# Kernel optimization log

Hardware: AMD Instinct MI355X
Metric: run time of the kernel (lower is better)

## Reference

```python
import jax, jax.numpy as jnp
import numpy as np
from jax import lax

H = W = 128          # feature map size (gen_line_map uses 128x128)
C = 128              # dim_loi
NPTS0 = 32           # n_pts0 samples per line
NPTS1 = 8            # after MaxPool1d(4, stride=4)
TOPK = 50            # n_dyn_junc
SCALE = 5.0          # proposal_lines distance scale


def proposal_lines(md_maps, dis_maps, scale=SCALE):
    h, w = md_maps.shape[1], md_maps.shape[2]
    y0, x0 = jnp.meshgrid(jnp.arange(h, dtype=jnp.float32),
                          jnp.arange(w, dtype=jnp.float32), indexing='ij')
    md_ = (md_maps[0] - 0.5) * np.pi * 2
    st_ = md_maps[1] * np.pi / 2
    ed_ = -md_maps[2] * np.pi / 2
    cs_md, ss_md = jnp.cos(md_), jnp.sin(md_)
    cs_st = jnp.clip(jnp.cos(st_), 0.001, None)
    ss_st = jnp.clip(jnp.sin(st_), 0.001, None)
    cs_ed = jnp.clip(jnp.cos(ed_), 0.001, None)
    ss_ed = jnp.clip(jnp.sin(ed_), None, -0.001)
    y_st = ss_st / cs_st
    y_ed = ss_ed / cs_ed
    d = dis_maps[0] * scale
    x_st = (cs_md - ss_md * y_st) * d
    y_s = (ss_md + cs_md * y_st) * d
    x_ed = (cs_md - ss_md * y_ed) * d
    y_e = (ss_md + cs_md * y_ed) * d
    x_st_f = jnp.clip(x_st + x0, 0.0, w - 1)
    y_st_f = jnp.clip(y_s + y0, 0.0, h - 1)
    x_ed_f = jnp.clip(x_ed + x0, 0.0, w - 1)
    y_ed_f = jnp.clip(y_e + y0, 0.0, h - 1)
    return jnp.stack((x_st_f, y_st_f, x_ed_f, y_ed_f), axis=-1).reshape(-1, 4)


def pooling(feats, lines):
    # feats: [C, H, W]; lines: [N, 4]
    h, w = feats.shape[1], feats.shape[2]
    tspan = jnp.linspace(0.0, 1.0, NPTS0)[None, None, :]           # [1,1,32]
    U, V = lines[:, :2], lines[:, 2:]
    sp = U[:, :, None] * tspan + V[:, :, None] * (1 - tspan) - 0.5  # [N,2,32]
    sp = sp.transpose(0, 2, 1).reshape(-1, 2)                       # [N*32, 2]
    px, py = sp[:, 0], sp[:, 1]
    px0 = jnp.clip(jnp.floor(px), 0.0, w - 1)
    py0 = jnp.clip(jnp.floor(py), 0.0, h - 1)
    px1 = jnp.clip(px0 + 1, 0.0, w - 1)
    py1 = jnp.clip(py0 + 1, 0.0, h - 1)
    px0l, py0l = px0.astype(jnp.int32), py0.astype(jnp.int32)
    px1l, py1l = px1.astype(jnp.int32), py1.astype(jnp.int32)
    # bilinear gather-weight, fused in a single expression: [C, N*32]
    xp = (feats[:, py0l, px0l] * (py1 - py) * (px1 - px)
          + feats[:, py1l, px0l] * (py - py0) * (px1 - px)
          + feats[:, py0l, px1l] * (py1 - py) * (px - px0)
          + feats[:, py1l, px1l] * (py - py0) * (px - px0))
    xp = xp.reshape(C, -1, NPTS0).transpose(1, 0, 2)                # [N, C, 32]
    xp = xp.reshape(xp.shape[0], C, NPTS1, NPTS0 // NPTS1).max(-1)  # MaxPool1d(4,4)
    return xp.reshape(-1, NPTS1 * C)                                # [N, 1024]


def nms(a):
    # F.max_pool2d(a, 3, stride=1, padding=1) then keep local maxima
    ap = lax.reduce_window(a, -jnp.inf, lax.max, (1, 3, 3), (1, 1, 1), 'SAME')
    return a * (a == ap).astype(a.dtype)


def get_junctions(jloc_nms, joff, topk=TOPK):
    h, w = jloc_nms.shape[1], jloc_nms.shape[2]
    scores, index = lax.top_k(jloc_nms.reshape(-1), topk)
    jf = joff.reshape(2, -1)
    y = (index // w).astype(jnp.float32) + jf[1][index] + 0.5
    x = (index % w).astype(jnp.float32) + jf[0][index] + 0.5
    juncs = jnp.stack((x, y), axis=1)                               # [topk, 2]
    return juncs, scores, index


def setup_inputs() -> dict:
    key = jax.random.key(0)
    ks = jax.random.split(key, 12)
    return {
        'md': jax.random.uniform(ks[0], (3, H, W), dtype=jnp.float32),
        'dis': jax.random.uniform(ks[1], (1, H, W), dtype=jnp.float32),
        'res': jax.random.uniform(ks[2], (1, H, W), dtype=jnp.float32),
        'jloc': jax.random.uniform(ks[3], (1, H, W), dtype=jnp.float32),
        'joff': jax.random.uniform(ks[4], (2, H, W), dtype=jnp.float32) - 0.5,
        'feats': jax.random.normal(ks[5], (C, H, W), dtype=jnp.float32),
        'W1': jax.random.normal(ks[6], (1024, C * NPTS1), dtype=jnp.float32) * 0.02,
        'b1': jax.random.normal(ks[7], (1024,), dtype=jnp.float32) * 0.02,
        'W2': jax.random.normal(ks[8], (1024, 1024), dtype=jnp.float32) * 0.02,
        'b2': jax.random.normal(ks[9], (1024,), dtype=jnp.float32) * 0.02,
        'W3': jax.random.normal(ks[10], (1, 1024), dtype=jnp.float32) * 0.02,
        'b3': jax.random.normal(ks[11], (1,), dtype=jnp.float32) * 0.02,
    }


def reference(md, dis, res, jloc, joff, feats, W1, b1, W2, b2, W3, b3):
    # line proposals at 3 residual scales (use_residual=True)
    lines = jnp.concatenate([
        proposal_lines(md, dis + s * res) for s in (-1.0, 0.0, 1.0)
    ], axis=0)                                                      # [3*H*W, 4]
    # LOI bilinear pooling + scoring MLP (self.fc)
    x = pooling(feats, lines)                                       # [N, 1024]
    x = jax.nn.relu(x @ W1.T + b1)
    x = jax.nn.relu(x @ W2.T + b2)
    logits = x @ W3.T + b3                                          # [N, 1]
    # junction decode: NMS + topk + offset gather
    juncs, jscores, _ = get_junctions(nms(jloc), joff, TOPK)
    return logits, juncs, jscores
```

## Files before the change

kernel.cpp:

```cpp
#include <hip/hip_runtime.h>
#include <hip/hip_bf16.h>
#include <math.h>

#define HH 128
#define WW 128
#define HW 16384
#define NL 49152
#define CC 128
#define NPTS0 32
#define NPTS1 8
#define PI_F 3.14159265358979323846f

typedef __attribute__((ext_vector_type(8))) short short8;
typedef __attribute__((ext_vector_type(4))) float f32x4;

__device__ __forceinline__ ushort f2bf(float f) {
    unsigned u = __builtin_bit_cast(unsigned, f);
    unsigned rounding = 0x7FFFu + ((u >> 16) & 1u);
    return (ushort)((u + rounding) >> 16);
}

__device__ __forceinline__ void gload_lds16(const void* gsrc, void* ldst) {
    __builtin_amdgcn_global_load_lds(
        (const __attribute__((address_space(1))) unsigned int*)gsrc,
        (__attribute__((address_space(3))) unsigned int*)ldst,
        16, 0, 0);
}

__device__ __forceinline__ void unpk8(uint4 d, float* f) {
    f[0] = __builtin_bit_cast(float, d.x << 16);
    f[1] = __builtin_bit_cast(float, d.x & 0xFFFF0000u);
    f[2] = __builtin_bit_cast(float, d.y << 16);
    f[3] = __builtin_bit_cast(float, d.y & 0xFFFF0000u);
    f[4] = __builtin_bit_cast(float, d.z << 16);
    f[5] = __builtin_bit_cast(float, d.z & 0xFFFF0000u);
    f[6] = __builtin_bit_cast(float, d.w << 16);
    f[7] = __builtin_bit_cast(float, d.w & 0xFFFF0000u);
}

__global__ __launch_bounds__(256) void k_lines(
    const float* __restrict__ md, const float* __restrict__ dis,
    const float* __restrict__ res, float* __restrict__ lines)
{
    int g = blockIdx.x * 256 + threadIdx.x;
    if (g >= NL) return;
    int s = g / HW;
    int pix = g - s * HW;
    float sf = (float)(s - 1);
    int y = pix >> 7, x = pix & 127;

    float md0 = md[pix], md1 = md[HW + pix], md2 = md[2 * HW + pix];
    float d = (dis[pix] + sf * res[pix]) * 5.0f;

    float md_ = (md0 - 0.5f) * (2.0f * PI_F);
    float st_ = md1 * (0.5f * PI_F);
    float ed_ = -md2 * (0.5f * PI_F);
    float cs_md = cosf(md_), ss_md = sinf(md_);
    float cs_st = fmaxf(cosf(st_), 0.001f);
    float ss_st = fmaxf(sinf(st_), 0.001f);
    float cs_ed = fmaxf(cosf(ed_), 0.001f);
    float ss_ed = fminf(sinf(ed_), -0.001f);
    float y_st = ss_st / cs_st;
    float y_ed = ss_ed / cs_ed;
    float x_st = (cs_md - ss_md * y_st) * d;
    float y_s  = (ss_md + cs_md * y_st) * d;
    float x_ed = (cs_md - ss_md * y_ed) * d;
    float y_e  = (ss_md + cs_md * y_ed) * d;

    float4 o;
    o.x = fminf(fmaxf(x_st + (float)x, 0.0f), 127.0f);
    o.y = fminf(fmaxf(y_s  + (float)y, 0.0f), 127.0f);
    o.z = fminf(fmaxf(x_ed + (float)x, 0.0f), 127.0f);
    o.w = fminf(fmaxf(y_e  + (float)y, 0.0f), 127.0f);
    ((float4*)lines)[g] = o;
}

__global__ void k_transpose(const float* __restrict__ in, ushort* __restrict__ out)
{
    __shared__ float tile[32][33];
    int cb = blockIdx.x;
    int pb = blockIdx.y;
    int tx = threadIdx.x, ty = threadIdx.y;
#pragma unroll
    for (int j = 0; j < 32; j += 8)
        tile[ty + j][tx] = in[(size_t)(cb * 32 + ty + j) * HW + pb * 32 + tx];
    __syncthreads();
#pragma unroll
    for (int j = 0; j < 32; j += 8)
        out[(size_t)(pb * 32 + ty + j) * CC + cb * 32 + tx] = f2bf(tile[tx][ty + j]);
}

__global__ void k_cvt(const float* __restrict__ a, const float* __restrict__ b,
                      ushort* __restrict__ oa, ushort* __restrict__ ob, int n)
{
    int i = blockIdx.x * 256 + threadIdx.x;
    if (i < n) { oa[i] = f2bf(a[i]); ob[i] = f2bf(b[i]); }
}

__global__ __launch_bounds__(128, 4) void k_pool(
    const ushort* __restrict__ ft, const float* __restrict__ lines,
    ushort* __restrict__ X)
{
    __shared__ __align__(16) unsigned smeta[2048];
    const int t = threadIdx.x;
    const int l_loc = t >> 4, c8 = t & 15;
    const int gl0 = blockIdx.x * 8;

#pragma unroll
    for (int e = 0; e < 2; ++e) {
        int s = t + e * 128;
        int ml = s >> 5, sp = s & 31;
        float4 L = ((const float4*)lines)[gl0 + ml];
        float tf = (float)sp * (1.0f / 31.0f);
        float omt = 1.0f - tf;
        float px = L.x * tf + L.z * omt - 0.5f;
        float py = L.y * tf + L.w * omt - 0.5f;
        float px0 = fminf(fmaxf(floorf(px), 0.0f), 127.0f);
        float py0 = fminf(fmaxf(floorf(py), 0.0f), 127.0f);
        float px1 = fminf(px0 + 1.0f, 127.0f);
        float py1 = fminf(py0 + 1.0f, 127.0f);
        int ix0 = (int)px0, iy0 = (int)py0, ix1 = (int)px1, iy1 = (int)py1;
        float4 wv;
        wv.x = (py1 - py) * (px1 - px);
        wv.y = (py  - py0) * (px1 - px);
        wv.z = (py1 - py) * (px  - px0);
        wv.w = (py  - py0) * (px  - px0);
        int o00 = (iy0 * WW + ix0) * (CC * 2);
        int dx  = (ix1 - ix0) * (CC * 2);
        int dy  = (iy1 - iy0) * (WW * CC * 2);
        int4 ov;
        ov.x = o00;
        ov.y = o00 + dy;
        ov.z = o00 + dx;
        ov.w = o00 + dy + dx;
        *(float4*)&smeta[s * 8]     = wv;
        *(int4*)  &smeta[s * 8 + 4] = ov;
    }
    __syncthreads();

    const unsigned coff = (unsigned)(c8 * 16);
    const char* fbase = (const char*)ft;
    float m[8][8];
#pragma unroll
    for (int ch = 0; ch < 8; ++ch)
#pragma unroll
        for (int g = 0; g < 8; ++g) m[ch][g] = -INFINITY;

#pragma unroll
    for (int g = 0; g < 8; ++g) {
#pragma unroll
        for (int j = 0; j < 4; ++j) {
            const unsigned* mp = &smeta[(l_loc * 32 + g * 4 + j) * 8];
            float4 wv = *(const float4*)mp;
            int4  ov = *(const int4*)(mp + 4);
            uint4 d00 = *(const uint4*)(fbase + ((unsigned)ov.x + coff));
            uint4 d10 = *(const uint4*)(fbase + ((unsigned)ov.y + coff));
            uint4 d01 = *(const uint4*)(fbase + ((unsigned)ov.z + coff));
            uint4 d11 = *(const uint4*)(fbase + ((unsigned)ov.w + coff));
            float f00[8], f10[8], f01[8], f11[8];
            unpk8(d00, f00); unpk8(d10, f10); unpk8(d01, f01); unpk8(d11, f11);
#pragma unroll
            for (int ch = 0; ch < 8; ++ch) {
                float v = f00[ch] * wv.x + f10[ch] * wv.y
                        + f01[ch] * wv.z + f11[ch] * wv.w;
                m[ch][g] = fmaxf(m[ch][g], v);
            }
        }
    }

    ushort* Xp = X + (size_t)(gl0 + l_loc) * 1024 + c8 * 64;
#pragma unroll
    for (int ch = 0; ch < 8; ++ch) {
        short8 pk;
#pragma unroll
        for (int g = 0; g < 8; ++g) pk[g] = (short)f2bf(m[ch][g]);
        *(short8*)(Xp + ch * 8) = pk;
    }
}

#define NT 32
template<int EPI>
__global__ __launch_bounds__(512, 2) void k_gemm2(
    const ushort* __restrict__ A, const ushort* __restrict__ B,
    const float* __restrict__ bias, ushort* __restrict__ Y,
    const float* __restrict__ w3, float* __restrict__ logits,
    int M, int N, int K)
{
    __shared__ __align__(16) ushort lds[65536];
    const int tid = threadIdx.x;
    const int w = tid >> 6, l = tid & 63;
    const int lr = l & 15, kq = l >> 4;
    const int wm = w >> 2, wn = w & 3;

    const int nwg = gridDim.x;
    const int cpx = nwg >> 3;
    const int swz = (blockIdx.x & 7) * cpx + (blockIdx.x >> 3);
    const int nbm = M >> 8;
    const int m_blk = swz % nbm;
    const int n_blk = swz / nbm;
    const int m0 = m_blk << 8, n0 = n_blk << 8;

    const int G0 = tid, G1 = 512 + tid;
    const int r0 = G0 >> 2, r1 = G1 >> 2;
    const int g0 = (G0 & 3) ^ ((r0 >> 1) & 3);
    const int g1 = (G1 & 3) ^ ((r1 >> 1) & 3);
    const ushort* sA0 = A + (size_t)(m0 + r0) * K + g0 * 8;
    const ushort* sA1 = A + (size_t)(m0 + r1) * K + g1 * 8;
    const ushort* sB0 = B + (size_t)(n0 + r0) * K + g0 * 8;
    const ushort* sB1 = B + (size_t)(n0 + r1) * K + g1 * 8;
    ushort* dA0 = &lds[G0 * 8];
    ushort* dA1 = &lds[G1 * 8];
    ushort* dB0 = &lds[32768 + G0 * 8];
    ushort* dB1 = &lds[32768 + G1 * 8];

#define STAGE_A(tp) { int sb = ((tp) & 3) * 8192; \
    gload_lds16(sA0 + (tp) * 32, dA0 + sb); \
    gload_lds16(sA1 + (tp) * 32, dA1 + sb); }
#define STAGE_B(tp) { int sb = ((tp) & 3) * 8192; \
    gload_lds16(sB0 + (tp) * 32, dB0 + sb); \
    gload_lds16(sB1 + (tp) * 32, dB1 + sb); }
#define SBAR  { __builtin_amdgcn_sched_barrier(0); __builtin_amdgcn_s_barrier(); \
                __builtin_amdgcn_sched_barrier(0); }

    int aidx[8], bidx[4];
#pragma unroll
    for (int m = 0; m < 8; ++m) {
        int r = wm * 128 + m * 16 + lr;
        int g = kq ^ ((r >> 1) & 3);
        aidx[m] = r * 32 + g * 8;
    }
#pragma unroll
    for (int n = 0; n < 4; ++n) {
        int r = wn * 64 + n * 16 + lr;
        int g = kq ^ ((r >> 1) & 3);
        bidx[n] = 32768 + r * 32 + g * 8;
    }

    f32x4 acc[8][4] = {};

    STAGE_A(0); STAGE_B(0); STAGE_A(1); STAGE_B(1); STAGE_A(2);
    asm volatile("s_waitcnt vmcnt(6)" ::: "memory");
    SBAR;

    for (int t = 0; t < NT; ++t) {
        const int sb = (t & 3) * 8192;
        short8 bq0 = *(const short8*)&lds[sb + bidx[0]];
        short8 bq1 = *(const short8*)&lds[sb + bidx[1]];
        short8 bq2 = *(const short8*)&lds[sb + bidx[2]];
        short8 bq3 = *(const short8*)&lds[sb + bidx[3]];
        short8 a0 = *(const short8*)&lds[sb + aidx[0]];
        short8 a1 = *(const short8*)&lds[sb + aidx[1]];
        short8 a2 = *(const short8*)&lds[sb + aidx[2]];
        short8 a3 = *(const short8*)&lds[sb + aidx[3]];
        if (t + 2 < NT) STAGE_B(t + 2);
        __builtin_amdgcn_s_setprio(1);
#pragma unroll
        for (int n = 0; n < 4; ++n) {
            short8 bn = (n == 0) ? bq0 : (n == 1) ? bq1 : (n == 2) ? bq2 : bq3;
            acc[0][n] = __builtin_amdgcn_mfma_f32_16x16x32_bf16(a0, bn, acc[0][n], 0, 0, 0);
            acc[1][n] = __builtin_amdgcn_mfma_f32_16x16x32_bf16(a1, bn, acc[1][n], 0, 0, 0);
            acc[2][n] = __builtin_amdgcn_mfma_f32_16x16x32_bf16(a2, bn, acc[2][n], 0, 0, 0);
            acc[3][n] = __builtin_amdgcn_mfma_f32_16x16x32_bf16(a3, bn, acc[3][n], 0, 0, 0);
        }
        __builtin_amdgcn_s_setprio(0);
        SBAR;
        short8 a4 = *(const short8*)&lds[sb + aidx[4]];
        short8 a5 = *(const short8*)&lds[sb + aidx[5]];
        short8 a6 = *(const short8*)&lds[sb + aidx[6]];
        short8 a7 = *(const short8*)&lds[sb + aidx[7]];
        if (t + 3 < NT) STAGE_A(t + 3);
        __builtin_amdgcn_s_setprio(1);
#pragma unroll
        for (int n = 0; n < 4; ++n) {
            short8 bn = (n == 0) ? bq0 : (n == 1) ? bq1 : (n == 2) ? bq2 : bq3;
            acc[4][n] = __builtin_amdgcn_mfma_f32_16x16x32_bf16(a4, bn, acc[4][n], 0, 0, 0);
            acc[5][n] = __builtin_amdgcn_mfma_f32_16x16x32_bf16(a5, bn, acc[5][n], 0, 0, 0);
            acc[6][n] = __builtin_amdgcn_mfma_f32_16x16x32_bf16(a6, bn, acc[6][n], 0, 0, 0);
            acc[7][n] = __builtin_amdgcn_mfma_f32_16x16x32_bf16(a7, bn, acc[7][n], 0, 0, 0);
        }
        __builtin_amdgcn_s_setprio(0);
        if (t < NT - 3) {
            asm volatile("s_waitcnt vmcnt(6)" ::: "memory");
        } else {
            asm volatile("s_waitcnt vmcnt(0)" ::: "memory");
        }
        SBAR;
    }
#undef STAGE_A
#undef STAGE_B
#undef SBAR

    if (EPI == 0) {
        float bv[4];
#pragma unroll
        for (int n = 0; n < 4; ++n) bv[n] = bias[n0 + wn * 64 + n * 16 + lr];
#pragma unroll
        for (int m = 0; m < 8; ++m) {
#pragma unroll
            for (int n = 0; n < 4; ++n) {
                int col = n0 + wn * 64 + n * 16 + lr;
#pragma unroll
                for (int j = 0; j < 4; ++j) {
                    int row = m0 + wm * 128 + m * 16 + kq * 4 + j;
                    float v = fmaxf(acc[m][n][j] + bv[n], 0.0f);
                    Y[(size_t)row * N + col] = f2bf(v);
                }
            }
        }
    } else {
        float w3v[4], bv[4];
#pragma unroll
        for (int n = 0; n < 4; ++n) {
            int col = n0 + wn * 64 + n * 16 + lr;
            w3v[n] = w3[col];
            bv[n] = bias[col];
        }
#pragma unroll
        for (int m = 0; m < 8; ++m) {
#pragma unroll
            for (int j = 0; j < 4; ++j) {
                float s = 0.0f;
#pragma unroll
                for (int n = 0; n < 4; ++n)
                    s += fmaxf(acc[m][n][j] + bv[n], 0.0f) * w3v[n];
#pragma unroll
                for (int off = 1; off < 16; off <<= 1)
                    s += __shfl_xor(s, off, 64);
                if (lr == 0)
                    atomicAdd(&logits[m0 + wm * 128 + m * 16 + kq * 4 + j], s);
            }
        }
    }
}

__global__ void k_init_logits(float* __restrict__ logits, const float* __restrict__ b3, int n)
{
    int i = blockIdx.x * 256 + threadIdx.x;
    if (i < n) logits[i] = b3[0];
}

__global__ __launch_bounds__(256) void k_nms_topk(
    const float* __restrict__ jloc, unsigned long long* __restrict__ cand)
{
    __shared__ unsigned long long sk[256];
    const int t = threadIdx.x;
    const int idx = blockIdx.x * 256 + t;
    const int y = idx >> 7, x = idx & 127;
    float cv = jloc[idx];
    float m = cv;
    for (int dy = -1; dy <= 1; ++dy) {
        int yy = y + dy;
        if (yy < 0 || yy > 127) continue;
        for (int dx = -1; dx <= 1; ++dx) {
            int xx = x + dx;
            if (xx < 0 || xx > 127) continue;
            m = fmaxf(m, jloc[(yy << 7) + xx]);
        }
    }
    float nv = (cv == m) ? cv : 0.0f;
    unsigned vb = __builtin_bit_cast(unsigned, nv);
    sk[t] = ((unsigned long long)vb << 32) | (unsigned)(0xFFFFFFFFu - idx);
    __syncthreads();
    for (int k = 2; k <= 256; k <<= 1) {
        for (int j = k >> 1; j >= 1; j >>= 1) {
            int ixj = t ^ j;
            if (ixj > t) {
                unsigned long long a = sk[t], b = sk[ixj];
                bool up = ((t & k) == 0);
                if (up ? (a < b) : (a > b)) { sk[t] = b; sk[ixj] = a; }
            }
            __syncthreads();
        }
    }
    if (t < 64) cand[blockIdx.x * 64 + t] = (t < 50) ? sk[t] : 0ull;
}

__global__ __launch_bounds__(1024) void k_topk_final(
    const unsigned long long* __restrict__ cand,
    const float* __restrict__ joff, float* __restrict__ outj)
{
    __shared__ unsigned long long sk[4096];
    const int t = threadIdx.x;
#pragma unroll
    for (int e = 0; e < 4; ++e) sk[t + (e << 10)] = cand[t + (e << 10)];
    __syncthreads();
    for (int k = 2; k <= 4096; k <<= 1) {
        for (int j = k >> 1; j >= 1; j >>= 1) {
#pragma unroll
            for (int e = 0; e < 4; ++e) {
                int i = t + (e << 10);
                int ixj = i ^ j;
                if (ixj > i) {
                    unsigned long long a = sk[i], b = sk[ixj];
                    bool up = ((i & k) == 0);
                    if (up ? (a < b) : (a > b)) { sk[i] = b; sk[ixj] = a; }
                }
            }
            __syncthreads();
        }
    }
    if (t < 50) {
        unsigned long long kk = sk[t];
        unsigned idx = 0xFFFFFFFFu - (unsigned)(kk & 0xFFFFFFFFull);
        float val = __builtin_bit_cast(float, (unsigned)(kk >> 32));
        int y = idx >> 7, x = idx & 127;
        outj[2 * t]     = (float)x + joff[idx]      + 0.5f;
        outj[2 * t + 1] = (float)y + joff[HW + idx] + 0.5f;
        outj[100 + t]   = val;
    }
}

extern "C" void kernel_launch(void* const* d_in, const int* in_sizes, int n_in,
                              void* d_out, int out_size, void* d_ws, size_t ws_size,
                              hipStream_t stream) {
    const float* md   = (const float*)d_in[0];
    const float* dis  = (const float*)d_in[1];
    const float* res  = (const float*)d_in[2];
    const float* jloc = (const float*)d_in[3];
    const float* joff = (const float*)d_in[4];
    const float* feats= (const float*)d_in[5];
    const float* W1   = (const float*)d_in[6];
    const float* b1   = (const float*)d_in[7];
    const float* W2   = (const float*)d_in[8];
    const float* b2   = (const float*)d_in[9];
    const float* W3   = (const float*)d_in[10];
    const float* b3   = (const float*)d_in[11];
    float* out = (float*)d_out;

    char* ws = (char*)d_ws;
    size_t off = 0;
    auto alloc = [&](size_t bytes) {
        void* p = ws + off;
        off = (off + bytes + 255) & ~(size_t)255;
        return p;
    };
    float*  lines = (float*) alloc((size_t)NL * 4 * sizeof(float));
    ushort* ft    = (ushort*)alloc((size_t)HW * CC * 2);
    ushort* W1b   = (ushort*)alloc((size_t)1024 * 1024 * 2);
    ushort* W2b   = (ushort*)alloc((size_t)1024 * 1024 * 2);
    ushort* X     = (ushort*)alloc((size_t)NL * 1024 * 2);
    ushort* Y1    = (ushort*)alloc((size_t)NL * 1024 * 2);
    unsigned long long* cand = (unsigned long long*)alloc(4096 * 8);

    k_lines<<<NL / 256, 256, 0, stream>>>(md, dis, res, lines);
    k_transpose<<<dim3(CC / 32, HW / 32), dim3(32, 8), 0, stream>>>(feats, ft);
    k_cvt<<<(1024 * 1024) / 256, 256, 0, stream>>>(W1, W2, W1b, W2b, 1024 * 1024);
    k_pool<<<NL / 8, 128, 0, stream>>>(ft, lines, X);

    int ngrid = (NL / 256) * (1024 / 256);
    k_gemm2<0><<<ngrid, 512, 0, stream>>>(X, W1b, b1, Y1, nullptr, nullptr, NL, 1024, 1024);
    k_init_logits<<<NL / 256, 256, 0, stream>>>(out, b3, NL);
    k_gemm2<1><<<ngrid, 512, 0, stream>>>(Y1, W2b, b2, nullptr, W3, out, NL, 1024, 1024);

    k_nms_topk<<<64, 256, 0, stream>>>(jloc, cand);
    k_topk_final<<<1, 1024, 0, stream>>>(cand, joff, out + NL);
}
```

Baseline: 374.5 us.

## Swap MFMA operands for row-major vector stores and merge split-phase MMA loop

Swaps the A and B operands of the MFMA so each lane's accumulator holds four consecutive output columns for one row. The epilogue can then write packed 4-element bf16 stores and load bias and w3 as float4. The logits reduction shrinks from a 16-lane shuffle tree per element to two shuffles per row. The main loop also drops the mid-iteration barrier and split A loads: all eight A fragments are loaded at once and both stages are issued before one MFMA block. This raises register pressure and changes how LDS reads overlap with the barrier-protected buffer reuse.

```diff
diff --git a/kernel.cpp b/kernel.cpp
--- a/kernel.cpp
+++ b/kernel.cpp
@@ -213,12 +213,12 @@
     ushort* dB0 = &lds[32768 + G0 * 8];
     ushort* dB1 = &lds[32768 + G1 * 8];
 
-#define STAGE_A(tp) { int sb = ((tp) & 3) * 8192; \
-    gload_lds16(sA0 + (tp) * 32, dA0 + sb); \
-    gload_lds16(sA1 + (tp) * 32, dA1 + sb); }
-#define STAGE_B(tp) { int sb = ((tp) & 3) * 8192; \
-    gload_lds16(sB0 + (tp) * 32, dB0 + sb); \
-    gload_lds16(sB1 + (tp) * 32, dB1 + sb); }
+#define STAGE_A(tp) { int sb_ = ((tp) & 3) * 8192; \
+    gload_lds16(sA0 + (tp) * 32, dA0 + sb_); \
+    gload_lds16(sA1 + (tp) * 32, dA1 + sb_); }
+#define STAGE_B(tp) { int sb_ = ((tp) & 3) * 8192; \
+    gload_lds16(sB0 + (tp) * 32, dB0 + sb_); \
+    gload_lds16(sB1 + (tp) * 32, dB1 + sb_); }
 #define SBAR  { __builtin_amdgcn_sched_barrier(0); __builtin_amdgcn_s_barrier(); \
                 __builtin_amdgcn_sched_barrier(0); }
 
@@ -248,35 +248,19 @@
         short8 bq1 = *(const short8*)&lds[sb + bidx[1]];
         short8 bq2 = *(const short8*)&lds[sb + bidx[2]];
         short8 bq3 = *(const short8*)&lds[sb + bidx[3]];
-        short8 a0 = *(const short8*)&lds[sb + aidx[0]];
-        short8 a1 = *(const short8*)&lds[sb + aidx[1]];
-        short8 a2 = *(const short8*)&lds[sb + aidx[2]];
-        short8 a3 = *(const short8*)&lds[sb + aidx[3]];
+        short8 a[8];
+#pragma unroll
+        for (int m = 0; m < 8; ++m)
+            a[m] = *(const short8*)&lds[sb + aidx[m]];
         if (t + 2 < NT) STAGE_B(t + 2);
-        __builtin_amdgcn_s_setprio(1);
-#pragma unroll
-        for (int n = 0; n < 4; ++n) {
-            short8 bn = (n == 0) ? bq0 : (n == 1) ? bq1 : (n == 2) ? bq2 : bq3;
-            acc[0][n] = __builtin_amdgcn_mfma_f32_16x16x32_bf16(a0, bn, acc[0][n], 0, 0, 0);
-            acc[1][n] = __builtin_amdgcn_mfma_f32_16x16x32_bf16(a1, bn, acc[1][n], 0, 0, 0);
-            acc[2][n] = __builtin_amdgcn_mfma_f32_16x16x32_bf16(a2, bn, acc[2][n], 0, 0, 0);
-            acc[3][n] = __builtin_amdgcn_mfma_f32_16x16x32_bf16(a3, bn, acc[3][n], 0, 0, 0);
-        }
-        __builtin_amdgcn_s_setprio(0);
-        SBAR;
-        short8 a4 = *(const short8*)&lds[sb + aidx[4]];
-        short8 a5 = *(const short8*)&lds[sb + aidx[5]];
-        short8 a6 = *(const short8*)&lds[sb + aidx[6]];
-        short8 a7 = *(const short8*)&lds[sb + aidx[7]];
         if (t + 3 < NT) STAGE_A(t + 3);
         __builtin_amdgcn_s_setprio(1);
 #pragma unroll
-        for (int n = 0; n < 4; ++n) {
-            short8 bn = (n == 0) ? bq0 : (n == 1) ? bq1 : (n == 2) ? bq2 : bq3;
-            acc[4][n] = __builtin_amdgcn_mfma_f32_16x16x32_bf16(a4, bn, acc[4][n], 0, 0, 0);
-            acc[5][n] = __builtin_amdgcn_mfma_f32_16x16x32_bf16(a5, bn, acc[5][n], 0, 0, 0);
-            acc[6][n] = __builtin_amdgcn_mfma_f32_16x16x32_bf16(a6, bn, acc[6][n], 0, 0, 0);
-            acc[7][n] = __builtin_amdgcn_mfma_f32_16x16x32_bf16(a7, bn, acc[7][n], 0, 0, 0);
+        for (int m = 0; m < 8; ++m) {
+            acc[m][0] = __builtin_amdgcn_mfma_f32_16x16x32_bf16(bq0, a[m], acc[m][0], 0, 0, 0);
+            acc[m][1] = __builtin_amdgcn_mfma_f32_16x16x32_bf16(bq1, a[m], acc[m][1], 0, 0, 0);
+            acc[m][2] = __builtin_amdgcn_mfma_f32_16x16x32_bf16(bq2, a[m], acc[m][2], 0, 0, 0);
+            acc[m][3] = __builtin_amdgcn_mfma_f32_16x16x32_bf16(bq3, a[m], acc[m][3], 0, 0, 0);
         }
         __builtin_amdgcn_s_setprio(0);
         if (t < NT - 3) {
@@ -291,44 +275,43 @@
 #undef SBAR
 
     if (EPI == 0) {
-        float bv[4];
-#pragma unroll
-        for (int n = 0; n < 4; ++n) bv[n] = bias[n0 + wn * 64 + n * 16 + lr];
+#pragma unroll
+        for (int n = 0; n < 4; ++n) {
+            int cbase = n0 + wn * 64 + n * 16 + kq * 4;
+            float4 bv4 = *(const float4*)&bias[cbase];
+#pragma unroll
+            for (int m = 0; m < 8; ++m) {
+                int row = m0 + wm * 128 + m * 16 + lr;
+                ushort4 pk;
+                pk.x = f2bf(fmaxf(acc[m][n][0] + bv4.x, 0.0f));
+                pk.y = f2bf(fmaxf(acc[m][n][1] + bv4.y, 0.0f));
+                pk.z = f2bf(fmaxf(acc[m][n][2] + bv4.z, 0.0f));
+                pk.w = f2bf(fmaxf(acc[m][n][3] + bv4.w, 0.0f));
+                *(ushort4*)(Y + (size_t)row * N + cbase) = pk;
+            }
+        }
+    } else {
+        float4 bv4[4], w34[4];
+#pragma unroll
+        for (int n = 0; n < 4; ++n) {
+            int cbase = n0 + wn * 64 + n * 16 + kq * 4;
+            bv4[n] = *(const float4*)&bias[cbase];
+            w34[n] = *(const float4*)&w3[cbase];
+        }
 #pragma unroll
         for (int m = 0; m < 8; ++m) {
+            float s = 0.0f;
 #pragma unroll
             for (int n = 0; n < 4; ++n) {
-                int col = n0 + wn * 64 + n * 16 + lr;
-#pragma unroll
-                for (int j = 0; j < 4; ++j) {
-                    int row = m0 + wm * 128 + m * 16 + kq * 4 + j;
-                    float v = fmaxf(acc[m][n][j] + bv[n], 0.0f);
-                    Y[(size_t)row * N + col] = f2bf(v);
-                }
+                s += fmaxf(acc[m][n][0] + bv4[n].x, 0.0f) * w34[n].x;
+                s += fmaxf(acc[m][n][1] + bv4[n].y, 0.0f) * w34[n].y;
+                s += fmaxf(acc[m][n][2] + bv4[n].z, 0.0f) * w34[n].z;
+                s += fmaxf(acc[m][n][3] + bv4[n].w, 0.0f) * w34[n].w;
             }
-        }
-    } else {
-        float w3v[4], bv[4];
-#pragma unroll
-        for (int n = 0; n < 4; ++n) {
-            int col = n0 + wn * 64 + n * 16 + lr;
-            w3v[n] = w3[col];
-            bv[n] = bias[col];
-        }
-#pragma unroll
-        for (int m = 0; m < 8; ++m) {
-#pragma unroll
-            for (int j = 0; j < 4; ++j) {
-                float s = 0.0f;
-#pragma unroll
-                for (int n = 0; n < 4; ++n)
-                    s += fmaxf(acc[m][n][j] + bv[n], 0.0f) * w3v[n];
-#pragma unroll
-                for (int off = 1; off < 16; off <<= 1)
-                    s += __shfl_xor(s, off, 64);
-                if (lr == 0)
-                    atomicAdd(&logits[m0 + wm * 128 + m * 16 + kq * 4 + j], s);
-            }
+            s += __shfl_xor(s, 16, 64);
+            s += __shfl_xor(s, 32, 64);
+            if (kq == 0)
+                atomicAdd(&logits[m0 + wm * 128 + m * 16 + lr], s);
         }
     }
 }
```

Result: no change. 370.4 us (-1.1%).
